# Performance work log

Hardware: AMD Instinct MI355X
Metric: run time of the kernel (lower is better)

The kernel has to match this reference:

```python
import jax, jax.numpy as jnp
import numpy as np

D_MODEL = 2048
N_HEADS = 16
D_HEAD = 128
D_LATENT = 512


def setup_inputs() -> dict:
    key = jax.random.key(0)
    ks = jax.random.split(key, 5)
    s = lambda fan_in: 1.0 / np.sqrt(fan_in)
    x = jax.random.normal(ks[0], (2, 2048, D_MODEL), dtype=jnp.float32)
    # nn.Linear weights stored as [out, in]; we keep [in, out] for x @ W
    W_q = jax.random.uniform(ks[1], (D_MODEL, N_HEADS * D_HEAD), jnp.float32, -s(D_MODEL), s(D_MODEL))
    W_kv_down = jax.random.uniform(ks[2], (D_MODEL, D_LATENT), jnp.float32, -s(D_MODEL), s(D_MODEL))
    W_kv_up = jax.random.uniform(ks[3], (D_LATENT, N_HEADS * D_HEAD), jnp.float32, -s(D_LATENT), s(D_LATENT))
    W_o = jax.random.uniform(ks[4], (N_HEADS * D_HEAD, D_MODEL), jnp.float32, -s(N_HEADS * D_HEAD), s(N_HEADS * D_HEAD))
    return {"x": x, "W_q": W_q, "W_kv_down": W_kv_down, "W_kv_up": W_kv_up, "W_o": W_o}


def reference(x, W_q, W_kv_down, W_kv_up, W_o):
    B, S, _ = x.shape
    # q: [B, H, S, Dh]
    q = (x @ W_q).reshape(B, S, N_HEADS, D_HEAD).transpose(0, 2, 1, 3)
    # latent compression then up-projection; shared K = V
    latent = x @ W_kv_down                      # [B, S, Dl]
    kv = (latent @ W_kv_up).reshape(B, S, N_HEADS, D_HEAD).transpose(0, 2, 1, 3)
    scale = 1.0 / np.sqrt(D_HEAD).astype(np.float32)
    scores = jnp.einsum('bhqd,bhkd->bhqk', q, kv) * scale  # [B,H,S,S]
    probs = jax.nn.softmax(scores, axis=-1)
    out = jnp.einsum('bhqk,bhkd->bhqd', probs, kv)          # [B,H,S,Dh]
    out = out.transpose(0, 2, 1, 3).reshape(B, S, N_HEADS * D_HEAD)
    return out @ W_o
```

## Files before the change

### kernel.cpp

```cpp
#include <hip/hip_runtime.h>

typedef __attribute__((ext_vector_type(8))) __bf16 bf16x8;
typedef __attribute__((ext_vector_type(4))) float f32x4;
typedef __attribute__((ext_vector_type(8))) unsigned short u16x8;
typedef __attribute__((ext_vector_type(4))) unsigned short u16x4;

#define MFMA16(a, b, c) __builtin_amdgcn_mfma_f32_16x16x32_bf16((a), (b), (c), 0, 0, 0)

__device__ __forceinline__ unsigned short f2bf(float f) {
    unsigned int u = __float_as_uint(f);
    unsigned int r = (u + 0x7FFFu + ((u >> 16) & 1u)) >> 16;
    return (unsigned short)r;
}

__device__ __forceinline__ void transpose_tile(const float* __restrict__ in,
                                               unsigned short* __restrict__ out,
                                               int R, int C, int bx, int by) {
    __shared__ float tile[32][33];
    const int tx = threadIdx.x & 31, ty = threadIdx.x >> 5;
    const int c0 = bx * 32, r0 = by * 32;
#pragma unroll
    for (int i = 0; i < 4; ++i)
        tile[ty + i * 8][tx] = in[(size_t)(r0 + ty + i * 8) * C + c0 + tx];
    __syncthreads();
#pragma unroll
    for (int i = 0; i < 4; ++i)
        out[(size_t)(c0 + ty + i * 8) * R + r0 + tx] = f2bf(tile[tx][ty + i * 8]);
}

__global__ __launch_bounds__(256) void k_prep(const float* __restrict__ x,
                                              const float* __restrict__ Wq,
                                              const float* __restrict__ Wkvd,
                                              const float* __restrict__ Wkvu,
                                              const float* __restrict__ Wo,
                                              unsigned short* __restrict__ xb,
                                              unsigned short* __restrict__ Wcat_t,
                                              unsigned short* __restrict__ Wkvu_t,
                                              unsigned short* __restrict__ Wo_t) {
    const int i = blockIdx.x;
    if (i < 8192) {
        const int idx = i * 256 + threadIdx.x;
        const float4 v = ((const float4*)x)[idx];
        u16x4 o = { f2bf(v.x), f2bf(v.y), f2bf(v.z), f2bf(v.w) };
        ((u16x4*)xb)[idx] = o;
    } else if (i < 12288) {
        const int j = i - 8192;
        transpose_tile(Wq, Wcat_t, 2048, 2048, j & 63, j >> 6);
    } else if (i < 13312) {
        const int j = i - 12288;
        transpose_tile(Wkvd, Wcat_t + 2048 * 2048, 2048, 512, j & 15, j >> 4);
    } else if (i < 14336) {
        const int j = i - 13312;
        transpose_tile(Wkvu, Wkvu_t, 512, 2048, j & 63, j >> 6);
    } else {
        const int j = i - 14336;
        transpose_tile(Wo, Wo_t, 2048, 2048, j & 63, j >> 6);
    }
}

template <int OUT_MODE>
__global__ __launch_bounds__(256) void k_gemm_bt(const unsigned short* __restrict__ A,
                                                 const unsigned short* __restrict__ B,
                                                 void* __restrict__ Cv,
                                                 unsigned short* __restrict__ Ct,
                                                 int M, int N, int K, float alpha) {
    __shared__ alignas(16) unsigned short As[2 * 128 * 32];
    __shared__ alignas(16) unsigned short Bs[2 * 128 * 32];
    const int tid = threadIdx.x;
    const int wave = tid >> 6;
    const int lane = tid & 63;
    const int l16 = lane & 15;
    const int quad = lane >> 4;
    const int bm = blockIdx.x * 128;
    const int bn = blockIdx.y * 128;
    const int wm = (wave >> 1) * 64;
    const int wn = (wave & 1) * 64;

    const f32x4 fzero = {0.f, 0.f, 0.f, 0.f};
    f32x4 acc[4][4];
#pragma unroll
    for (int i = 0; i < 4; ++i)
#pragma unroll
        for (int j = 0; j < 4; ++j) acc[i][j] = fzero;

    auto AsL = (__attribute__((address_space(3))) unsigned short*)As;
    auto BsL = (__attribute__((address_space(3))) unsigned short*)Bs;

    const int c0 = wave * 128 + lane;

    auto stage = [&](int kt32) {
        const int boff = (kt32 & 1) * (128 * 32);
        const int kt = kt32 * 32;
#pragma unroll
        for (int j = 0; j < 2; ++j) {
            const int c = c0 + j * 64;
            __builtin_amdgcn_global_load_lds(
                (const __attribute__((address_space(1))) void*)(A + (size_t)(bm + (c >> 2)) * K + kt + (c & 3) * 8),
                (__attribute__((address_space(3))) void*)(AsL + boff + c * 8), 16, 0, 0);
            __builtin_amdgcn_global_load_lds(
                (const __attribute__((address_space(1))) void*)(B + (size_t)(bn + (c >> 2)) * K + kt + (c & 3) * 8),
                (__attribute__((address_space(3))) void*)(BsL + boff + c * 8), 16, 0, 0);
        }
    };

    const int nk = K >> 5;
    stage(0);
    for (int kt32 = 0; kt32 < nk; ++kt32) {
        __syncthreads();
        if (kt32 + 1 < nk) stage(kt32 + 1);
        const unsigned short* Ab = As + (kt32 & 1) * (128 * 32);
        const unsigned short* Bb = Bs + (kt32 & 1) * (128 * 32);

        bf16x8 af[4], bfr[4];
#pragma unroll
        for (int mt = 0; mt < 4; ++mt)
            af[mt] = *(const bf16x8*)(Ab + (wm + mt * 16 + l16) * 32 + quad * 8);
#pragma unroll
        for (int nt = 0; nt < 4; ++nt)
            bfr[nt] = *(const bf16x8*)(Bb + (wn + nt * 16 + l16) * 32 + quad * 8);
#pragma unroll
        for (int mt = 0; mt < 4; ++mt)
#pragma unroll
            for (int nt = 0; nt < 4; ++nt)
                acc[mt][nt] = MFMA16(af[mt], bfr[nt], acc[mt][nt]);
    }

#pragma unroll
    for (int mt = 0; mt < 4; ++mt)
#pragma unroll
        for (int nt = 0; nt < 4; ++nt) {
            const int row0 = bm + wm + mt * 16 + quad * 4;
            const int col = bn + wn + nt * 16 + l16;
            u16x4 pk;
#pragma unroll
            for (int r = 0; r < 4; ++r) {
                const float v0 = acc[mt][nt][r];
                if (OUT_MODE == 0) {
                    ((float*)Cv)[(size_t)(row0 + r) * N + col] = v0 * alpha;
                } else if (OUT_MODE == 3) {
                    if (col < 2048)
                        ((unsigned short*)Cv)[(size_t)(row0 + r) * 2048 + col] = f2bf(v0 * alpha);
                    else
                        Ct[(size_t)(row0 + r) * 512 + (col - 2048)] = f2bf(v0);
                } else {
                    const unsigned short b = f2bf(v0 * alpha);
                    ((unsigned short*)Cv)[(size_t)(row0 + r) * N + col] = b;
                    pk[r] = b;
                }
            }
            if (OUT_MODE == 2) {
                const size_t ti =
                    ((size_t)((row0 >> 11) * (N >> 7) + (col >> 7)) * 128 + (col & 127)) * 2048 +
                    (row0 & 2047);
                *(u16x4*)(Ct + ti) = pk;
            }
        }
}

__global__ __launch_bounds__(256, 2) void k_attn(const unsigned short* __restrict__ Q,
                                                 const unsigned short* __restrict__ KV,
                                                 const unsigned short* __restrict__ KVT,
                                                 unsigned short* __restrict__ O) {
    __shared__ alignas(16) unsigned short Ks[2 * 64 * 128];
    __shared__ alignas(16) unsigned short Vt[2 * 128 * 64];
    __shared__ alignas(16) unsigned short Ps[4 * 32 * 64];

    const int tid = threadIdx.x;
    const int wave = tid >> 6, lane = tid & 63;
    const int l16 = lane & 15, quad = lane >> 4;
    const int l8 = l16 & 7;
    const int qt = blockIdx.x;
    const int bh = blockIdx.y;
    const size_t tokbase = (size_t)(bh >> 4) * 2048;
    const int hcol = (bh & 15) * 128;
    const unsigned short* kvt_head = KVT + (size_t)bh * (128 * 2048);

    bf16x8 qf[2][4];
    const int qrow0 = qt * 128 + wave * 32;
#pragma unroll
    for (int nt = 0; nt < 2; ++nt) {
        const unsigned short* qp =
            Q + (tokbase + qrow0 + nt * 16 + l16) * 2048 + hcol + quad * 8;
#pragma unroll
        for (int kd = 0; kd < 4; ++kd) qf[nt][kd] = *(const bf16x8*)(qp + kd * 32);
    }

    const f32x4 fzero = {0.f, 0.f, 0.f, 0.f};
    f32x4 o_acc[8][2];
#pragma unroll
    for (int dt = 0; dt < 8; ++dt)
#pragma unroll
        for (int nt = 0; nt < 2; ++nt) o_acc[dt][nt] = fzero;
    float l_i[2] = {0.f, 0.f};

    const int krow = tid >> 4, kchunk = tid & 15;
    const int vrow = tid >> 3, vchunk = tid & 7;

    unsigned short* Pw = Ps + wave * (32 * 64);

    u16x8 kR[4], vR[4];
    auto load_tile = [&](int kt) {
#pragma unroll
        for (int p = 0; p < 4; ++p) {
            kR[p] = *(const u16x8*)(KV + (tokbase + kt * 64 + p * 16 + krow) * 2048 +
                                    hcol + kchunk * 8);
            vR[p] = *(const u16x8*)(kvt_head + (size_t)(p * 32 + vrow) * 2048 + kt * 64 +
                                    vchunk * 8);
        }
    };
    auto store_tile = [&](int kt) {
        unsigned short* Kb = Ks + (kt & 1) * (64 * 128);
        unsigned short* Vb = Vt + (kt & 1) * (128 * 64);
#pragma unroll
        for (int p = 0; p < 4; ++p) {
            const int r = p * 16 + krow;
            const int swk = (kchunk & 8) | ((kchunk & 7) ^ (r & 7));
            *(u16x8*)(Kb + r * 128 + swk * 8) = kR[p];
            const int d = p * 32 + vrow;
            const int swv = vchunk ^ (d & 7);
            *(u16x8*)(Vb + d * 64 + swv * 8) = vR[p];
        }
    };

    load_tile(0);
    store_tile(0);
    load_tile(1);

    for (int kt = 0; kt < 32; ++kt) {
        __syncthreads();
        if (kt < 31) {
            store_tile(kt + 1);
            if (kt < 30) load_tile(kt + 2);
        }
        const unsigned short* Kb = Ks + (kt & 1) * (64 * 128);
        const unsigned short* Vb = Vt + (kt & 1) * (128 * 64);

        f32x4 st[4][2];
#pragma unroll
        for (int mt = 0; mt < 4; ++mt)
#pragma unroll
            for (int nt = 0; nt < 2; ++nt) st[mt][nt] = fzero;
#pragma unroll
        for (int kd = 0; kd < 4; ++kd)
#pragma unroll
            for (int mt = 0; mt < 4; ++mt) {
                const int c = kd * 4 + quad;
                const int sw = (c & 8) | ((c & 7) ^ l8);
                const bf16x8 kf = *(const bf16x8*)(Kb + (mt * 16 + l16) * 128 + sw * 8);
                st[mt][0] = MFMA16(kf, qf[0][kd], st[mt][0]);
                st[mt][1] = MFMA16(kf, qf[1][kd], st[mt][1]);
            }

#pragma unroll
        for (int nt = 0; nt < 2; ++nt) {
            float rs = 0.f;
            unsigned short* prow = Pw + (nt * 16 + l16) * 64;
#pragma unroll
            for (int mt = 0; mt < 4; ++mt) {
                u16x4 pk;
#pragma unroll
                for (int r = 0; r < 4; ++r) {
                    const float p = __expf(st[mt][nt][r]);
                    rs += p;
                    pk[r] = f2bf(p);
                }
                const int c = mt * 2 + (quad >> 1);
                *(u16x4*)(prow + (c ^ l8) * 8 + (quad & 1) * 4) = pk;
            }
            rs += __shfl_xor(rs, 16);
            rs += __shfl_xor(rs, 32);
            l_i[nt] += rs;
        }

        __builtin_amdgcn_sched_barrier(0);

#pragma unroll
        for (int s = 0; s < 2; ++s) {
            const int c = s * 4 + quad;
            const int sw = (c ^ l8) * 8;
            bf16x8 pfr[2];
#pragma unroll
            for (int nt = 0; nt < 2; ++nt)
                pfr[nt] = *(const bf16x8*)(Pw + (nt * 16 + l16) * 64 + sw);
#pragma unroll
            for (int dt = 0; dt < 8; ++dt) {
                const bf16x8 vf = *(const bf16x8*)(Vb + (dt * 16 + l16) * 64 + sw);
                o_acc[dt][0] = MFMA16(vf, pfr[0], o_acc[dt][0]);
                o_acc[dt][1] = MFMA16(vf, pfr[1], o_acc[dt][1]);
            }
        }
    }

#pragma unroll
    for (int nt = 0; nt < 2; ++nt) {
        const float inv = 1.0f / l_i[nt];
        unsigned short* dst = O + (tokbase + qrow0 + nt * 16 + l16) * 2048 + hcol;
#pragma unroll
        for (int dt = 0; dt < 8; ++dt) {
            u16x4 pk;
#pragma unroll
            for (int r = 0; r < 4; ++r) pk[r] = f2bf(o_acc[dt][nt][r] * inv);
            *(u16x4*)(dst + dt * 16 + quad * 4) = pk;
        }
    }
}

extern "C" void kernel_launch(void* const* d_in, const int* in_sizes, int n_in,
                              void* d_out, int out_size, void* d_ws, size_t ws_size,
                              hipStream_t stream) {
    const float* x = (const float*)d_in[0];
    const float* W_q = (const float*)d_in[1];
    const float* W_kvd = (const float*)d_in[2];
    const float* W_kvu = (const float*)d_in[3];
    const float* W_o = (const float*)d_in[4];

    char* w = (char*)d_ws;
    unsigned short* xb = (unsigned short*)(w);
    unsigned short* kvT = xb;
    unsigned short* qb = (unsigned short*)(w + (size_t)16 * 1024 * 1024);
    unsigned short* kvb = (unsigned short*)(w + (size_t)32 * 1024 * 1024);
    unsigned short* Wo_t = (unsigned short*)(w + (size_t)48 * 1024 * 1024);
    unsigned short* Wcat_t = (unsigned short*)(w + (size_t)56 * 1024 * 1024);
    unsigned short* Wkvu_t = (unsigned short*)(w + (size_t)66 * 1024 * 1024);
    unsigned short* lat = (unsigned short*)(w + (size_t)68 * 1024 * 1024);

    k_prep<<<18432, 256, 0, stream>>>(x, W_q, W_kvd, W_kvu, W_o, xb, Wcat_t, Wkvu_t, Wo_t);

    k_gemm_bt<3><<<dim3(32, 20), 256, 0, stream>>>(xb, Wcat_t, qb, lat, 4096, 2560, 2048,
                                                   0.08838834764831845f);
    k_gemm_bt<2><<<dim3(32, 16), 256, 0, stream>>>(lat, Wkvu_t, kvb, kvT, 4096, 2048, 512,
                                                   1.0f);
    k_attn<<<dim3(16, 32), 256, 0, stream>>>(qb, kvb, kvT, qb);
    k_gemm_bt<0><<<dim3(32, 16), 256, 0, stream>>>(qb, Wo_t, d_out, nullptr, 4096, 2048, 2048,
                                                   1.0f);
}
```

Baseline: 318.3 us.

## Keep softmax probabilities in registers via permlane swaps instead of LDS round-trip

Replaces the per-wave LDS staging of the bf16 probability tile with an in-register layout conversion using v_permlane32_swap/v_permlane16_swap and packed v_cvt_pk_bf16_f32 conversions. The row-sum reduction also uses permlane swaps instead of shuffles. The block index is remapped so that neighbouring workgroups are spread across batch-head groups. This removes the LDS write/read and the scheduling barrier from the inner loop. In exchange it adds permlane instructions and depends on the operand layout being mapped correctly.

```diff
diff --git a/kernel.cpp b/kernel.cpp
--- a/kernel.cpp
+++ b/kernel.cpp
@@ -4,6 +4,8 @@
 typedef __attribute__((ext_vector_type(4))) float f32x4;
 typedef __attribute__((ext_vector_type(8))) unsigned short u16x8;
 typedef __attribute__((ext_vector_type(4))) unsigned short u16x4;
+typedef __attribute__((ext_vector_type(2))) unsigned int u32x2;
+typedef __attribute__((ext_vector_type(4))) unsigned int u32x4;
 
 #define MFMA16(a, b, c) __builtin_amdgcn_mfma_f32_16x16x32_bf16((a), (b), (c), 0, 0, 0)
 
@@ -11,6 +13,32 @@
     unsigned int u = __float_as_uint(f);
     unsigned int r = (u + 0x7FFFu + ((u >> 16) & 1u)) >> 16;
     return (unsigned short)r;
+}
+
+__device__ __forceinline__ u32x2 plswap32(unsigned int x, unsigned int y) {
+#if __has_builtin(__builtin_amdgcn_permlane32_swap)
+    return __builtin_amdgcn_permlane32_swap(x, y, false, false);
+#else
+    asm volatile("s_nop 1\n\tv_permlane32_swap_b32 %0, %1" : "+v"(x), "+v"(y));
+    u32x2 r = {x, y};
+    return r;
+#endif
+}
+__device__ __forceinline__ u32x2 plswap16(unsigned int x, unsigned int y) {
+#if __has_builtin(__builtin_amdgcn_permlane16_swap)
+    return __builtin_amdgcn_permlane16_swap(x, y, false, false);
+#else
+    asm volatile("s_nop 1\n\tv_permlane16_swap_b32 %0, %1" : "+v"(x), "+v"(y));
+    u32x2 r = {x, y};
+    return r;
+#endif
+}
+
+__device__ __forceinline__ float quad_reduce(float v) {
+    u32x2 a = plswap32(__float_as_uint(v), __float_as_uint(v));
+    v = __uint_as_float(a.x) + __uint_as_float(a.y);
+    u32x2 b = plswap16(__float_as_uint(v), __float_as_uint(v));
+    return __uint_as_float(b.x) + __uint_as_float(b.y);
 }
 
 __device__ __forceinline__ void transpose_tile(const float* __restrict__ in,
@@ -163,14 +191,15 @@
                                                  unsigned short* __restrict__ O) {
     __shared__ alignas(16) unsigned short Ks[2 * 64 * 128];
     __shared__ alignas(16) unsigned short Vt[2 * 128 * 64];
-    __shared__ alignas(16) unsigned short Ps[4 * 32 * 64];
 
     const int tid = threadIdx.x;
     const int wave = tid >> 6, lane = tid & 63;
     const int l16 = lane & 15, quad = lane >> 4;
     const int l8 = l16 & 7;
-    const int qt = blockIdx.x;
-    const int bh = blockIdx.y;
+    const int lid = blockIdx.x + (blockIdx.y << 4);
+    const int wid = ((lid & 7) << 6) + (lid >> 3);
+    const int qt = wid & 15;
+    const int bh = wid >> 4;
     const size_t tokbase = (size_t)(bh >> 4) * 2048;
     const int hcol = (bh & 15) * 128;
     const unsigned short* kvt_head = KVT + (size_t)bh * (128 * 2048);
@@ -195,8 +224,6 @@
 
     const int krow = tid >> 4, kchunk = tid & 15;
     const int vrow = tid >> 3, vchunk = tid & 7;
-
-    unsigned short* Pw = Ps + wave * (32 * 64);
 
     u16x8 kR[4], vR[4];
     auto load_tile = [&](int kt) {
@@ -251,42 +278,43 @@
                 st[mt][1] = MFMA16(kf, qf[1][kd], st[mt][1]);
             }
 
+        bf16x8 pfr[2][2];
 #pragma unroll
         for (int nt = 0; nt < 2; ++nt) {
+            float p[4][4];
             float rs = 0.f;
-            unsigned short* prow = Pw + (nt * 16 + l16) * 64;
-#pragma unroll
-            for (int mt = 0; mt < 4; ++mt) {
-                u16x4 pk;
+#pragma unroll
+            for (int mt = 0; mt < 4; ++mt)
 #pragma unroll
                 for (int r = 0; r < 4; ++r) {
-                    const float p = __expf(st[mt][nt][r]);
-                    rs += p;
-                    pk[r] = f2bf(p);
+                    p[mt][r] = __expf(st[mt][nt][r]);
+                    rs += p[mt][r];
                 }
-                const int c = mt * 2 + (quad >> 1);
-                *(u16x4*)(prow + (c ^ l8) * 8 + (quad & 1) * 4) = pk;
-            }
-            rs += __shfl_xor(rs, 16);
-            rs += __shfl_xor(rs, 32);
-            l_i[nt] += rs;
-        }
-
-        __builtin_amdgcn_sched_barrier(0);
+            l_i[nt] += quad_reduce(rs);
+#pragma unroll
+            for (int s = 0; s < 2; ++s) {
+                unsigned int aw0, aw1, bw0, bw1;
+                asm("v_cvt_pk_bf16_f32 %0, %1, %2" : "=v"(aw0) : "v"(p[2 * s][0]), "v"(p[2 * s][1]));
+                asm("v_cvt_pk_bf16_f32 %0, %1, %2" : "=v"(aw1) : "v"(p[2 * s][2]), "v"(p[2 * s][3]));
+                asm("v_cvt_pk_bf16_f32 %0, %1, %2" : "=v"(bw0) : "v"(p[2 * s + 1][0]), "v"(p[2 * s + 1][1]));
+                asm("v_cvt_pk_bf16_f32 %0, %1, %2" : "=v"(bw1) : "v"(p[2 * s + 1][2]), "v"(p[2 * s + 1][3]));
+                const u32x2 e0 = plswap32(aw0, bw0);
+                const u32x2 e1 = plswap32(aw1, bw1);
+                const u32x2 f0 = plswap16(e0.x, e0.y);
+                const u32x2 f1 = plswap16(e1.x, e1.y);
+                const u32x4 w = {f0.x, f1.x, f0.y, f1.y};
+                pfr[s][nt] = __builtin_bit_cast(bf16x8, w);
+            }
+        }
 
 #pragma unroll
         for (int s = 0; s < 2; ++s) {
-            const int c = s * 4 + quad;
-            const int sw = (c ^ l8) * 8;
-            bf16x8 pfr[2];
-#pragma unroll
-            for (int nt = 0; nt < 2; ++nt)
-                pfr[nt] = *(const bf16x8*)(Pw + (nt * 16 + l16) * 64 + sw);
+            const int sw = ((s * 4 + quad) ^ l8) * 8;
 #pragma unroll
             for (int dt = 0; dt < 8; ++dt) {
                 const bf16x8 vf = *(const bf16x8*)(Vb + (dt * 16 + l16) * 64 + sw);
-                o_acc[dt][0] = MFMA16(vf, pfr[0], o_acc[dt][0]);
-                o_acc[dt][1] = MFMA16(vf, pfr[1], o_acc[dt][1]);
+                o_acc[dt][0] = MFMA16(vf, pfr[s][0], o_acc[dt][0]);
+                o_acc[dt][1] = MFMA16(vf, pfr[s][1], o_acc[dt][1]);
             }
         }
     }
```

New measurement: 309.4 us. -2.8%, faster.
